# Kernel tuning notes

Hardware: AMD Instinct MI355X
Metric: run time of the kernel (lower is better)

## Reference

```python
import jax, jax.numpy as jnp
import numpy as np

B, P, Q, H = 8, 2048, 512, 1024


def setup_inputs() -> dict:
    key = jax.random.key(0)
    k1, k2, k3, k4, k5 = jax.random.split(key, 5)
    passage = jax.random.normal(k1, (B, P, H), dtype=jnp.float32)
    question = jax.random.normal(k2, (B, Q, H), dtype=jnp.float32)
    q_mask = jax.random.randint(k3, (B, Q), 0, 2, dtype=jnp.int32)
    # map_linear params (torch Linear: y = x @ W.T + b)
    bound = 1.0 / np.sqrt(H)
    map_W = jax.random.uniform(k4, (H, H), jnp.float32, -bound, bound)
    map_b = jax.random.uniform(k5, (H,), jnp.float32, -bound, bound)
    return {"passage": passage, "question": question, "q_mask": q_mask,
            "map_W": map_W, "map_b": map_b}


def reference(passage, question, q_mask, map_W, map_b):
    # scores: [B, P, Q]
    scores = jnp.einsum("bph,bqh->bpq", passage, question)
    mask = q_mask.astype(scores.dtype)[:, None, :]  # [B, 1, Q], broadcasts over P
    # multiplicative masked softmax + renormalize (memory_efficient=False path)
    a = jax.nn.softmax(scores * mask, axis=-1) * mask
    alpha = a / (jnp.sum(a, axis=-1, keepdims=True) + 1e-13)
    # attend: [B, P, H]
    out = jnp.einsum("bpq,bqh->bph", alpha, question)
    # fused linear + ReLU
    return jax.nn.relu(jnp.einsum("bph,oh->bpo", out, map_W) + map_b)
```

## Files before the change

### kernel.cpp

```cpp
#include <hip/hip_runtime.h>
#include <hip/hip_bf16.h>

typedef _Float16 f16;
typedef _Float16 f16x8 __attribute__((ext_vector_type(8)));
typedef _Float16 f16x4 __attribute__((ext_vector_type(4)));
typedef float f32x4 __attribute__((ext_vector_type(4)));
typedef int i32x4 __attribute__((ext_vector_type(4)));

#define B_ 8
#define P_ 2048
#define Q_ 512
#define H_ 1024

__device__ __forceinline__ void gload_lds16(const void* g, void* l) {
  __builtin_amdgcn_global_load_lds(
      (const __attribute__((address_space(1))) void*)g,
      (__attribute__((address_space(3))) void*)l, 16, 0, 0);
}

__global__ __launch_bounds__(256) void k_cvt16(const float* __restrict__ x,
                                               f16* __restrict__ y, int n4) {
  int i = blockIdx.x * blockDim.x + threadIdx.x;
  int stride = gridDim.x * blockDim.x;
  for (; i < n4; i += stride) {
    f32x4 v = ((const f32x4*)x)[i];
    f16x4 h;
#pragma unroll
    for (int j = 0; j < 4; ++j) h[j] = (f16)v[j];
    ((f16x4*)y)[i] = h;
  }
}

__global__ __launch_bounds__(256) void k_transpose(const float* __restrict__ q,
                                                   f16* __restrict__ qT,
                                                   f16* __restrict__ q16) {
  __shared__ float t[64][65];
  int b = blockIdx.z;
  int h0 = blockIdx.x * 64, q0 = blockIdx.y * 64;
  int tid = threadIdx.x;
  int c4 = (tid & 15) * 4;
  int r16 = tid >> 4;
  const float* src = q + ((long)b * Q_ + q0) * H_ + h0;
  f16* d16 = q16 + ((long)b * Q_ + q0) * H_ + h0;
#pragma unroll
  for (int i = 0; i < 4; ++i) {
    int r = r16 + i * 16;
    f32x4 v = *(const f32x4*)(src + (long)r * H_ + c4);
    f16x4 s;
#pragma unroll
    for (int j = 0; j < 4; ++j) s[j] = (f16)v[j];
    *(f16x4*)(d16 + (long)r * H_ + c4) = s;
    t[c4 + 0][r] = v[0];
    t[c4 + 1][r] = v[1];
    t[c4 + 2][r] = v[2];
    t[c4 + 3][r] = v[3];
  }
  __syncthreads();
  f16* dst = qT + ((long)b * H_ + h0) * Q_ + q0;
#pragma unroll
  for (int i = 0; i < 4; ++i) {
    int hr = r16 + i * 16;
    f16x4 o;
#pragma unroll
    for (int j = 0; j < 4; ++j) o[j] = (f16)t[hr][c4 + j];
    *(f16x4*)(dst + (long)hr * Q_ + c4) = o;
  }
}

__global__ __launch_bounds__(512, 2) void k_gemm1(
    const float* __restrict__ passage, const f16* __restrict__ q16,
    float* __restrict__ S) {
  constexpr int NT = H_ / 32;
  __shared__ __align__(16) f16 smem[40960];

  int orig = blockIdx.x;
  int wg = (orig & 7) * 32 + (orig >> 3);
  int bx = wg & 1, by = (wg >> 1) & 15, z = wg >> 5;
  int row0 = by * 128, col0 = bx * 256;

  int tid = threadIdx.x, wv = tid >> 6, lane = tid & 63;
  int fr = lane & 15, kq = lane >> 4;
  int wr = (wv >> 2) * 64, wc = (wv & 3) * 64;
  int swz = (kq ^ ((fr >> 1) & 3)) * 8;

  int ar = tid >> 2, ac = tid & 3;
  const float* gA = passage + ((long)(z * P_ + row0 + ar)) * H_ + ac * 8;
  int aw = ar * 32 + ((ac ^ ((ar >> 1) & 3)) * 8);

  const f16* gB = q16 + ((long)(z * Q_ + col0 + (tid >> 2))) * H_ +
                  (((tid & 3) ^ ((tid >> 3) & 3)) * 8);

  auto stageB = [&](int t) {
    const f16* g = gB + t * 32;
    f16* l = smem + 8192 + (t & 3) * 8192 + wv * 512;
    gload_lds16(g, l);
    gload_lds16(g + (long)128 * H_, l + 4096);
  };
  auto writeA = [&](int t, f32x4 lo, f32x4 hi) {
    f16x8 h;
#pragma unroll
    for (int j = 0; j < 4; ++j) {
      h[j] = (f16)lo[j];
      h[4 + j] = (f16)hi[j];
    }
    *(f16x8*)(smem + (t & 1) * 4096 + aw) = h;
  };

  f32x4 acc[4][4] = {};
  f32x4 a0lo, a0hi, a1lo, a1hi;

  a0lo = *(const f32x4*)(gA);
  a0hi = *(const f32x4*)(gA + 4);
  a1lo = *(const f32x4*)(gA + 32);
  a1hi = *(const f32x4*)(gA + 36);
  stageB(0);
  stageB(1);
  stageB(2);
  writeA(0, a0lo, a0hi);
  asm volatile("s_waitcnt vmcnt(4) lgkmcnt(0)" ::: "memory");
  __builtin_amdgcn_s_barrier();
  __builtin_amdgcn_sched_barrier(0);

#pragma unroll 4
  for (int t = 0; t < NT; ++t) {
    if (t + 2 < NT) {
      const float* g = gA + (t + 2) * 32;
      if (t & 1) {
        a1lo = *(const f32x4*)(g);
        a1hi = *(const f32x4*)(g + 4);
      } else {
        a0lo = *(const f32x4*)(g);
        a0hi = *(const f32x4*)(g + 4);
      }
    }
    if (t + 3 < NT) stageB(t + 3);
    f16x8 af[4], bf[4];
    const f16* Ab = smem + (t & 1) * 4096;
    const f16* Bb = smem + 8192 + (t & 3) * 8192;
#pragma unroll
    for (int m = 0; m < 4; ++m)
      af[m] = *(const f16x8*)(Ab + (wr + m * 16 + fr) * 32 + swz);
#pragma unroll
    for (int n = 0; n < 4; ++n)
      bf[n] = *(const f16x8*)(Bb + (wc + n * 16 + fr) * 32 + swz);
    if (t + 1 < NT)
      writeA(t + 1, (t & 1) ? a0lo : a1lo, (t & 1) ? a0hi : a1hi);
    __builtin_amdgcn_s_setprio(1);
#pragma unroll
    for (int m = 0; m < 4; ++m)
#pragma unroll
      for (int n = 0; n < 4; ++n)
        acc[m][n] = __builtin_amdgcn_mfma_f32_16x16x32_f16(af[m], bf[n],
                                                           acc[m][n], 0, 0, 0);
    __builtin_amdgcn_s_setprio(0);
    if (t <= NT - 4)
      asm volatile("s_waitcnt vmcnt(6) lgkmcnt(0)" ::: "memory");
    else if (t == NT - 3)
      asm volatile("s_waitcnt vmcnt(4) lgkmcnt(0)" ::: "memory");
    else
      asm volatile("s_waitcnt vmcnt(0) lgkmcnt(0)" ::: "memory");
    if (t < NT - 1) {
      __builtin_amdgcn_s_barrier();
      __builtin_amdgcn_sched_barrier(0);
    }
  }

  float* Sp = S + (long)z * P_ * Q_;
  int r0 = row0 + wr + (lane >> 4) * 4;
  int c0 = col0 + wc + fr;
#pragma unroll
  for (int m = 0; m < 4; ++m)
#pragma unroll
    for (int n = 0; n < 4; ++n)
#pragma unroll
      for (int j = 0; j < 4; ++j)
        Sp[(long)(r0 + m * 16 + j) * Q_ + c0 + n * 16] = acc[m][n][j];
}

__global__ __launch_bounds__(256) void k_softmax(const float* __restrict__ S,
                                                 const int* __restrict__ qmask,
                                                 f16* __restrict__ alpha) {
  int row = blockIdx.x * 4 + (threadIdx.x >> 6);
  int lane = threadIdx.x & 63;
  int b = row >> 11;
  const float* s = S + (long)row * Q_;
  const int* mp = qmask + b * Q_;
  f32x4 v0 = ((const f32x4*)s)[lane * 2];
  f32x4 v1 = ((const f32x4*)s)[lane * 2 + 1];
  i32x4 m0 = ((const i32x4*)mp)[lane * 2];
  i32x4 m1 = ((const i32x4*)mp)[lane * 2 + 1];
  float t[8], mf[8];
#pragma unroll
  for (int j = 0; j < 4; ++j) {
    mf[j] = (float)m0[j];     t[j] = v0[j] * mf[j];
    mf[4 + j] = (float)m1[j]; t[4 + j] = v1[j] * mf[4 + j];
  }
  float mx = t[0];
#pragma unroll
  for (int j = 1; j < 8; ++j) mx = fmaxf(mx, t[j]);
  for (int o = 32; o; o >>= 1) mx = fmaxf(mx, __shfl_xor(mx, o, 64));
  float e[8], Z = 0.f, Sm = 0.f;
#pragma unroll
  for (int j = 0; j < 8; ++j) {
    e[j] = expf(t[j] - mx);
    Z += e[j];
    Sm += e[j] * mf[j];
  }
  for (int o = 32; o; o >>= 1) {
    Z += __shfl_xor(Z, o, 64);
    Sm += __shfl_xor(Sm, o, 64);
  }
  float inv = 1.0f / (Sm + 1e-13f * Z);
  f16x8 out;
#pragma unroll
  for (int j = 0; j < 8; ++j) out[j] = (f16)(e[j] * mf[j] * inv);
  *(f16x8*)(alpha + (long)row * Q_ + lane * 8) = out;
}

template <int EPI, int NT>
__global__ __launch_bounds__(512, 2) void k_gemm256(
    const f16* __restrict__ A, const f16* __restrict__ Bm,
    void* __restrict__ Cv, const float* __restrict__ bias, int N, int gx,
    int gy, long sA, long sB, long sC) {
  constexpr int K = NT * 32;
  __shared__ __align__(16) f16 smem[65536];

  int nwg = gridDim.x;
  int orig = blockIdx.x;
  int wg = (orig & 7) * (nwg >> 3) + (orig >> 3);
  int bx = wg % gx;
  int tt = wg / gx;
  int by = tt % gy;
  int z = tt / gy;
  int row0 = by * 256, col0 = bx * 256;
  A += z * sA;
  Bm += z * sB;

  int tid = threadIdx.x, wv = tid >> 6, lane = tid & 63;

  bool isA = wv < 4;
  int u0 = (wv & 3) * 4;
  int srow = u0 * 16 + (lane >> 2);
  int sclog = ((lane & 3) ^ ((lane >> 3) & 3)) * 8;
  const f16* sbaseG = isA ? A + (long)(row0 + srow) * K + sclog
                          : Bm + (long)(col0 + srow) * K + sclog;
  int sbaseL = (isA ? 0 : 8192) + u0 * 512;

  auto stage = [&](int tile) {
    const f16* g = sbaseG + (long)tile * 32;
    f16* l = smem + (tile & 3) * 16384 + sbaseL;
#pragma unroll
    for (int j = 0; j < 4; ++j) gload_lds16(g + (long)j * 16 * K, l + j * 512);
  };

  int wr = (wv >> 2) * 128, wc = (wv & 3) * 64;
  int fr = lane & 15, kq = lane >> 4;
  int swz = (kq ^ ((fr >> 1) & 3)) * 8 + fr * 32;

  f32x4 acc[8][4] = {};
  auto compute = [&](int t) {
    const f16* bufA = smem + (t & 3) * 16384;
    const f16* bufB = bufA + 8192;
    f16x8 af[8], bfr[4];
#pragma unroll
    for (int m = 0; m < 8; ++m)
      af[m] = *(const f16x8*)(bufA + (wr + m * 16) * 32 + swz);
#pragma unroll
    for (int n = 0; n < 4; ++n)
      bfr[n] = *(const f16x8*)(bufB + (wc + n * 16) * 32 + swz);
#pragma unroll
    for (int m = 0; m < 8; ++m)
#pragma unroll
      for (int n = 0; n < 4; ++n)
        acc[m][n] = __builtin_amdgcn_mfma_f32_16x16x32_f16(af[m], bfr[n],
                                                           acc[m][n], 0, 0, 0);
  };

  stage(0);
  stage(1);
  stage(2);
  asm volatile("s_waitcnt vmcnt(8)" ::: "memory");
  __builtin_amdgcn_s_barrier();
  __builtin_amdgcn_sched_barrier(0);
  for (int t = 0; t < NT - 3; ++t) {
    stage(t + 3);
    compute(t);
    asm volatile("s_waitcnt vmcnt(8)" ::: "memory");
    __builtin_amdgcn_s_barrier();
    __builtin_amdgcn_sched_barrier(0);
  }
  compute(NT - 3);
  asm volatile("s_waitcnt vmcnt(4)" ::: "memory");
  __builtin_amdgcn_s_barrier();
  __builtin_amdgcn_sched_barrier(0);
  compute(NT - 2);
  asm volatile("s_waitcnt vmcnt(0)" ::: "memory");
  __builtin_amdgcn_s_barrier();
  __builtin_amdgcn_sched_barrier(0);
  compute(NT - 1);

  int r0 = row0 + wr + (lane >> 4) * 4;
  int c0 = col0 + wc + fr;
  if constexpr (EPI == 1) {
    f16* C = (f16*)Cv + z * sC;
#pragma unroll
    for (int m = 0; m < 8; ++m)
#pragma unroll
      for (int n = 0; n < 4; ++n)
#pragma unroll
        for (int j = 0; j < 4; ++j)
          C[(long)(r0 + m * 16 + j) * N + c0 + n * 16] = (f16)acc[m][n][j];
  } else {
    float* C = (float*)Cv;
#pragma unroll
    for (int n = 0; n < 4; ++n) {
      float bv = bias[c0 + n * 16];
#pragma unroll
      for (int m = 0; m < 8; ++m)
#pragma unroll
        for (int j = 0; j < 4; ++j) {
          float v = acc[m][n][j] + bv;
          __builtin_nontemporal_store(
              fmaxf(v, 0.f), &C[(long)(r0 + m * 16 + j) * N + c0 + n * 16]);
        }
    }
  }
}

extern "C" void kernel_launch(void* const* d_in, const int* in_sizes, int n_in,
                              void* d_out, int out_size, void* d_ws,
                              size_t ws_size, hipStream_t stream) {
  const float* passage = (const float*)d_in[0];
  const float* question = (const float*)d_in[1];
  const int* qmask = (const int*)d_in[2];
  const float* mapW = (const float*)d_in[3];
  const float* mapb = (const float*)d_in[4];

  char* ws = (char*)d_ws;
  size_t off = 0;
  auto alloc = [&](size_t bytes) {
    void* p = ws + off;
    off += (bytes + 255) & ~(size_t)255;
    return p;
  };
  f16* q16 = (f16*)alloc((size_t)B_ * Q_ * H_ * 2);
  f16* qT = (f16*)alloc((size_t)B_ * H_ * Q_ * 2);
  f16* w16 = (f16*)alloc((size_t)H_ * H_ * 2);
  f16* alpha = (f16*)alloc((size_t)B_ * P_ * Q_ * 2);
  f16* O = (f16*)alloc((size_t)B_ * P_ * H_ * 2);
  float* S = (float*)alloc((size_t)B_ * P_ * Q_ * 4);

  k_cvt16<<<512, 256, 0, stream>>>(mapW, w16, H_ * H_ / 4);
  k_transpose<<<dim3(H_ / 64, Q_ / 64, B_), 256, 0, stream>>>(question, qT,
                                                              q16);

  k_gemm1<<<256, 512, 0, stream>>>(passage, q16, S);

  k_softmax<<<B_ * P_ / 4, 256, 0, stream>>>(S, qmask, alpha);

  k_gemm256<1, Q_ / 32><<<256, 512, 0, stream>>>(
      alpha, qT, O, nullptr, H_, H_ / 256, P_ / 256, (long)P_ * Q_,
      (long)H_ * Q_, (long)P_ * H_);

  k_gemm256<2, H_ / 32><<<256, 512, 0, stream>>>(
      O, w16, d_out, mapb, H_, H_ / 256, (B_ * P_) / 256, 0, 0, 0);
}
```

Baseline: 118.1 us.

## Fuse partial masked softmax into score GEMM epilogue with split-row rescale

The score GEMM epilogue now computes a per-tile masked softmax: a row max reduced through LDS across the 256-column tile, the exponentials, and partial Z and masked sums. It writes unnormalized fp16 exponentials plus per-half-row (max, Z, Sm) partials instead of a full fp32 score matrix. A light rowscale kernel merges the two column-half partials and rescales alpha in place. This removes the fp32 S write and read (64MB each way) at the cost of extra epilogue syncs and LDS reductions in the GEMM. Storing unnormalized exponentials in fp16 before rescaling could change rounding slightly.

Result: slower. 123.5 us (+4.7%).

```diff
diff --git a/kernel.cpp b/kernel.cpp
--- a/kernel.cpp
+++ b/kernel.cpp
@@ -69,7 +69,8 @@
 
 __global__ __launch_bounds__(512, 2) void k_gemm1(
     const float* __restrict__ passage, const f16* __restrict__ q16,
-    float* __restrict__ S) {
+    const int* __restrict__ qmask, f16* __restrict__ alphaE,
+    float* __restrict__ part) {
   constexpr int NT = H_ / 32;
   __shared__ __align__(16) f16 smem[40960];
 
@@ -165,56 +166,102 @@
     }
   }
 
-  float* Sp = S + (long)z * P_ * Q_;
-  int r0 = row0 + wr + (lane >> 4) * 4;
-  int c0 = col0 + wc + fr;
+  __syncthreads();
+  float* red = (float*)smem;
+  float* red2 = red + 512;
+  const int* qm = qmask + z * Q_ + col0;
+  float mk[4];
+#pragma unroll
+  for (int n = 0; n < 4; ++n) mk[n] = (float)qm[wc + n * 16 + fr];
+
+  int rbase = wr + (lane >> 4) * 4;
+  float mxl[4][4];
 #pragma unroll
   for (int m = 0; m < 4; ++m)
 #pragma unroll
-    for (int n = 0; n < 4; ++n)
-#pragma unroll
-      for (int j = 0; j < 4; ++j)
-        Sp[(long)(r0 + m * 16 + j) * Q_ + c0 + n * 16] = acc[m][n][j];
-}
-
-__global__ __launch_bounds__(256) void k_softmax(const float* __restrict__ S,
-                                                 const int* __restrict__ qmask,
-                                                 f16* __restrict__ alpha) {
+    for (int j = 0; j < 4; ++j) {
+      float v = acc[m][0][j] * mk[0];
+#pragma unroll
+      for (int n = 1; n < 4; ++n) v = fmaxf(v, acc[m][n][j] * mk[n]);
+      v = fmaxf(v, __shfl_xor(v, 1, 64));
+      v = fmaxf(v, __shfl_xor(v, 2, 64));
+      v = fmaxf(v, __shfl_xor(v, 4, 64));
+      v = fmaxf(v, __shfl_xor(v, 8, 64));
+      if (fr == 0) red[(rbase + m * 16 + j) * 4 + (wv & 3)] = v;
+    }
+  __syncthreads();
+#pragma unroll
+  for (int m = 0; m < 4; ++m)
+#pragma unroll
+    for (int j = 0; j < 4; ++j) {
+      int r = rbase + m * 16 + j;
+      mxl[m][j] = fmaxf(fmaxf(red[r * 4], red[r * 4 + 1]),
+                        fmaxf(red[r * 4 + 2], red[r * 4 + 3]));
+    }
+#pragma unroll
+  for (int m = 0; m < 4; ++m)
+#pragma unroll
+    for (int j = 0; j < 4; ++j) {
+      float zs = 0.f, ss = 0.f;
+#pragma unroll
+      for (int n = 0; n < 4; ++n) {
+        float e = expf(acc[m][n][j] * mk[n] - mxl[m][j]);
+        acc[m][n][j] = e * mk[n];
+        zs += e;
+        ss += e * mk[n];
+      }
+      zs += __shfl_xor(zs, 1, 64); ss += __shfl_xor(ss, 1, 64);
+      zs += __shfl_xor(zs, 2, 64); ss += __shfl_xor(ss, 2, 64);
+      zs += __shfl_xor(zs, 4, 64); ss += __shfl_xor(ss, 4, 64);
+      zs += __shfl_xor(zs, 8, 64); ss += __shfl_xor(ss, 8, 64);
+      if (fr == 0) {
+        red2[((rbase + m * 16 + j) * 4 + (wv & 3)) * 2] = zs;
+        red2[((rbase + m * 16 + j) * 4 + (wv & 3)) * 2 + 1] = ss;
+      }
+    }
+  __syncthreads();
+  f16* ap = alphaE + ((long)(z * P_ + row0)) * Q_ + col0;
+#pragma unroll
+  for (int m = 0; m < 4; ++m)
+#pragma unroll
+    for (int j = 0; j < 4; ++j) {
+      int r = rbase + m * 16 + j;
+      if ((wv & 3) == 0 && fr == 0) {
+        float Z = 0.f, Sm = 0.f;
+#pragma unroll
+        for (int w = 0; w < 4; ++w) {
+          Z += red2[(r * 4 + w) * 2];
+          Sm += red2[(r * 4 + w) * 2 + 1];
+        }
+        float* pp = part + ((long)(z * 2 + bx) * P_ + row0 + r) * 4;
+        pp[0] = mxl[m][j];
+        pp[1] = Z;
+        pp[2] = Sm;
+      }
+#pragma unroll
+      for (int n = 0; n < 4; ++n)
+        ap[(long)r * Q_ + wc + n * 16 + fr] = (f16)acc[m][n][j];
+    }
+}
+
+__global__ __launch_bounds__(256) void k_rowscale(f16* __restrict__ alpha,
+                                                  const float* __restrict__ part) {
   int row = blockIdx.x * 4 + (threadIdx.x >> 6);
   int lane = threadIdx.x & 63;
-  int b = row >> 11;
-  const float* s = S + (long)row * Q_;
-  const int* mp = qmask + b * Q_;
-  f32x4 v0 = ((const f32x4*)s)[lane * 2];
-  f32x4 v1 = ((const f32x4*)s)[lane * 2 + 1];
-  i32x4 m0 = ((const i32x4*)mp)[lane * 2];
-  i32x4 m1 = ((const i32x4*)mp)[lane * 2 + 1];
-  float t[8], mf[8];
-#pragma unroll
-  for (int j = 0; j < 4; ++j) {
-    mf[j] = (float)m0[j];     t[j] = v0[j] * mf[j];
-    mf[4 + j] = (float)m1[j]; t[4 + j] = v1[j] * mf[4 + j];
-  }
-  float mx = t[0];
-#pragma unroll
-  for (int j = 1; j < 8; ++j) mx = fmaxf(mx, t[j]);
-  for (int o = 32; o; o >>= 1) mx = fmaxf(mx, __shfl_xor(mx, o, 64));
-  float e[8], Z = 0.f, Sm = 0.f;
-#pragma unroll
-  for (int j = 0; j < 8; ++j) {
-    e[j] = expf(t[j] - mx);
-    Z += e[j];
-    Sm += e[j] * mf[j];
-  }
-  for (int o = 32; o; o >>= 1) {
-    Z += __shfl_xor(Z, o, 64);
-    Sm += __shfl_xor(Sm, o, 64);
-  }
-  float inv = 1.0f / (Sm + 1e-13f * Z);
-  f16x8 out;
-#pragma unroll
-  for (int j = 0; j < 8; ++j) out[j] = (f16)(e[j] * mf[j] * inv);
-  *(f16x8*)(alpha + (long)row * Q_ + lane * 8) = out;
+  int z = row >> 11, pr = row & 2047;
+  const float* p0 = part + ((long)(z * 2 + 0) * P_ + pr) * 4;
+  const float* p1 = part + ((long)(z * 2 + 1) * P_ + pr) * 4;
+  float m0 = p0[0], Z0 = p0[1], S0 = p0[2];
+  float m1 = p1[0], Z1 = p1[1], S1 = p1[2];
+  float M = fmaxf(m0, m1);
+  float s0 = expf(m0 - M), s1 = expf(m1 - M);
+  float inv = 1.0f / (S0 * s0 + S1 * s1 + 1e-13f * (Z0 * s0 + Z1 * s1));
+  float sc = (lane < 32 ? s0 : s1) * inv;
+  f16* ap = alpha + (long)row * Q_ + lane * 8;
+  f16x8 v = *(f16x8*)ap;
+#pragma unroll
+  for (int j = 0; j < 8; ++j) v[j] = (f16)((float)v[j] * sc);
+  *(f16x8*)ap = v;
 }
 
 template <int EPI, int NT>
@@ -348,15 +395,15 @@
   f16* w16 = (f16*)alloc((size_t)H_ * H_ * 2);
   f16* alpha = (f16*)alloc((size_t)B_ * P_ * Q_ * 2);
   f16* O = (f16*)alloc((size_t)B_ * P_ * H_ * 2);
-  float* S = (float*)alloc((size_t)B_ * P_ * Q_ * 4);
+  float* part = (float*)alloc((size_t)B_ * 2 * P_ * 4 * 4);
 
   k_cvt16<<<512, 256, 0, stream>>>(mapW, w16, H_ * H_ / 4);
   k_transpose<<<dim3(H_ / 64, Q_ / 64, B_), 256, 0, stream>>>(question, qT,
                                                               q16);
 
-  k_gemm1<<<256, 512, 0, stream>>>(passage, q16, S);
-
-  k_softmax<<<B_ * P_ / 4, 256, 0, stream>>>(S, qmask, alpha);
+  k_gemm1<<<256, 512, 0, stream>>>(passage, q16, qmask, alpha, part);
+
+  k_rowscale<<<B_ * P_ / 4, 256, 0, stream>>>(alpha, part);
 
   k_gemm256<1, Q_ / 32><<<256, 512, 0, stream>>>(
       alpha, qT, O, nullptr, H_, H_ / 256, P_ / 256, (long)P_ * Q_,
```

## Restructure 256x256 GEMM to K=64 tiles with double buffering and prefetched fragments

Applied to the files above, without the earlier changes.

The 256x256 GEMM kernel now uses 64-wide K tiles with two LDS buffers instead of four 32-wide buffers, so there are half as many barriers per K loop. Each iteration loads all LDS fragments into registers first, waits, then issues the next stage's global-to-LDS loads so the buffer being read can be safely overwritten. The MFMA block runs under raised wave priority via s_setprio. The cost is a shallower prefetch (two stages instead of three) and more registers for the doubled fragments, which may reduce latency hiding or occupancy.

Result: slower. 151.6 us (+28.4%).

```diff
diff --git a/kernel.cpp b/kernel.cpp
--- a/kernel.cpp
+++ b/kernel.cpp
@@ -222,7 +222,7 @@
     const f16* __restrict__ A, const f16* __restrict__ Bm,
     void* __restrict__ Cv, const float* __restrict__ bias, int N, int gx,
     int gy, long sA, long sB, long sC) {
-  constexpr int K = NT * 32;
+  constexpr int K = NT * 64;
   __shared__ __align__(16) f16 smem[65536];
 
   int nwg = gridDim.x;
@@ -238,66 +238,79 @@
 
   int tid = threadIdx.x, wv = tid >> 6, lane = tid & 63;
 
-  bool isA = wv < 4;
-  int u0 = (wv & 3) * 4;
-  int srow = u0 * 16 + (lane >> 2);
-  int sclog = ((lane & 3) ^ ((lane >> 3) & 3)) * 8;
-  const f16* sbaseG = isA ? A + (long)(row0 + srow) * K + sclog
-                          : Bm + (long)(col0 + srow) * K + sclog;
-  int sbaseL = (isA ? 0 : 8192) + u0 * 512;
-
-  auto stage = [&](int tile) {
-    const f16* g = sbaseG + (long)tile * 32;
-    f16* l = smem + (tile & 3) * 16384 + sbaseL;
-#pragma unroll
-    for (int j = 0; j < 4; ++j) gload_lds16(g + (long)j * 16 * K, l + j * 512);
+  int rowR = tid >> 3;
+  int half = (tid >> 2) & 1;
+  int cl = (tid & 3) ^ ((rowR >> 1) & 3);
+  const f16* gAs = A + (long)(row0 + rowR) * K + half * 32 + cl * 8;
+  const f16* gBs = Bm + (long)(col0 + rowR) * K + half * 32 + cl * 8;
+
+  auto stage = [&](int t) {
+    f16* l = smem + (t & 1) * 32768 + tid * 8;
+    const f16* ga = gAs + (long)t * 64;
+    const f16* gb = gBs + (long)t * 64;
+#pragma unroll
+    for (int j = 0; j < 4; ++j)
+      gload_lds16(ga + (long)j * 64 * K, l + j * 4096);
+#pragma unroll
+    for (int j = 0; j < 4; ++j)
+      gload_lds16(gb + (long)j * 64 * K, l + 16384 + j * 4096);
   };
 
   int wr = (wv >> 2) * 128, wc = (wv & 3) * 64;
   int fr = lane & 15, kq = lane >> 4;
-  int swz = (kq ^ ((fr >> 1) & 3)) * 8 + fr * 32;
+  int swz = (kq ^ ((fr >> 1) & 3)) * 8;
 
   f32x4 acc[8][4] = {};
-  auto compute = [&](int t) {
-    const f16* bufA = smem + (t & 3) * 16384;
-    const f16* bufB = bufA + 8192;
-    f16x8 af[8], bfr[4];
-#pragma unroll
-    for (int m = 0; m < 8; ++m)
-      af[m] = *(const f16x8*)(bufA + (wr + m * 16) * 32 + swz);
-#pragma unroll
-    for (int n = 0; n < 4; ++n)
-      bfr[n] = *(const f16x8*)(bufB + (wc + n * 16) * 32 + swz);
-#pragma unroll
-    for (int m = 0; m < 8; ++m)
-#pragma unroll
-      for (int n = 0; n < 4; ++n)
-        acc[m][n] = __builtin_amdgcn_mfma_f32_16x16x32_f16(af[m], bfr[n],
-                                                           acc[m][n], 0, 0, 0);
-  };
 
   stage(0);
   stage(1);
-  stage(2);
   asm volatile("s_waitcnt vmcnt(8)" ::: "memory");
   __builtin_amdgcn_s_barrier();
   __builtin_amdgcn_sched_barrier(0);
-  for (int t = 0; t < NT - 3; ++t) {
-    stage(t + 3);
-    compute(t);
-    asm volatile("s_waitcnt vmcnt(8)" ::: "memory");
+#pragma unroll 2
+  for (int t = 0; t < NT; ++t) {
+    const f16* bufA = smem + (t & 1) * 32768;
+    const f16* bufB = bufA + 16384;
+    f16x8 af0[8], bf0[4], af1[8], bf1[4];
+#pragma unroll
+    for (int m = 0; m < 8; ++m)
+      af0[m] = *(const f16x8*)(bufA + (wr + m * 16 + fr) * 64 + swz);
+#pragma unroll
+    for (int n = 0; n < 4; ++n)
+      bf0[n] = *(const f16x8*)(bufB + (wc + n * 16 + fr) * 64 + swz);
+#pragma unroll
+    for (int m = 0; m < 8; ++m)
+      af1[m] = *(const f16x8*)(bufA + (wr + m * 16 + fr) * 64 + 32 + swz);
+#pragma unroll
+    for (int n = 0; n < 4; ++n)
+      bf1[n] = *(const f16x8*)(bufB + (wc + n * 16 + fr) * 64 + 32 + swz);
+    asm volatile("s_waitcnt lgkmcnt(0)" ::: "memory");
+    __builtin_amdgcn_sched_barrier(0);
     __builtin_amdgcn_s_barrier();
-    __builtin_amdgcn_sched_barrier(0);
-  }
-  compute(NT - 3);
-  asm volatile("s_waitcnt vmcnt(4)" ::: "memory");
-  __builtin_amdgcn_s_barrier();
-  __builtin_amdgcn_sched_barrier(0);
-  compute(NT - 2);
-  asm volatile("s_waitcnt vmcnt(0)" ::: "memory");
-  __builtin_amdgcn_s_barrier();
-  __builtin_amdgcn_sched_barrier(0);
-  compute(NT - 1);
+    if (t + 2 < NT) stage(t + 2);
+    __builtin_amdgcn_s_setprio(1);
+#pragma unroll
+    for (int m = 0; m < 8; ++m)
+#pragma unroll
+      for (int n = 0; n < 4; ++n)
+        acc[m][n] = __builtin_amdgcn_mfma_f32_16x16x32_f16(af0[m], bf0[n],
+                                                           acc[m][n], 0, 0, 0);
+#pragma unroll
+    for (int m = 0; m < 8; ++m)
+#pragma unroll
+      for (int n = 0; n < 4; ++n)
+        acc[m][n] = __builtin_amdgcn_mfma_f32_16x16x32_f16(af1[m], bf1[n],
+                                                           acc[m][n], 0, 0, 0);
+    __builtin_amdgcn_s_setprio(0);
+    if (t + 2 < NT)
+      asm volatile("s_waitcnt vmcnt(8)" ::: "memory");
+    else
+      asm volatile("s_waitcnt vmcnt(0)" ::: "memory");
+    if (t + 1 < NT) {
+      __builtin_amdgcn_s_barrier();
+      __builtin_amdgcn_sched_barrier(0);
+    }
+  }
 
   int r0 = row0 + wr + (lane >> 4) * 4;
   int c0 = col0 + wc + fr;
@@ -358,10 +371,10 @@
 
   k_softmax<<<B_ * P_ / 4, 256, 0, stream>>>(S, qmask, alpha);
 
-  k_gemm256<1, Q_ / 32><<<256, 512, 0, stream>>>(
+  k_gemm256<1, Q_ / 64><<<256, 512, 0, stream>>>(
       alpha, qT, O, nullptr, H_, H_ / 256, P_ / 256, (long)P_ * Q_,
       (long)H_ * Q_, (long)P_ * H_);
 
-  k_gemm256<2, H_ / 32><<<256, 512, 0, stream>>>(
+  k_gemm256<2, H_ / 64><<<256, 512, 0, stream>>>(
       O, w16, d_out, mapb, H_, H_ / 256, (B_ * P_) / 256, 0, 0, 0);
 }
```

## Shrink GEMM tiles to 256x128 with triple-buffered LDS and higher occupancy

Applied to the files above, without the earlier changes.

Changes the two f16 GEMMs from 256x256 to 256x128 output tiles, doubling the grid to 512 workgroups. The LDS pipeline drops from four 32 KB stages (three in flight) to three 24 KB slots (two in flight), and the launch-bounds occupancy hint rises from 2 to 4. s_setprio is raised around the MFMA block. Smaller tiles give more blocks and better wave occupancy across the 256 CUs, at the cost of lower arithmetic intensity per tile, more global and L2 traffic, and a shallower prefetch.

Result: no change. 119.4 us (+1.2%).

```diff
diff --git a/kernel.cpp b/kernel.cpp
--- a/kernel.cpp
+++ b/kernel.cpp
@@ -218,12 +218,13 @@
 }
 
 template <int EPI, int NT>
-__global__ __launch_bounds__(512, 2) void k_gemm256(
+__global__ __launch_bounds__(512, 4) void k_gemm256(
     const f16* __restrict__ A, const f16* __restrict__ Bm,
     void* __restrict__ Cv, const float* __restrict__ bias, int N, int gx,
     int gy, long sA, long sB, long sC) {
   constexpr int K = NT * 32;
-  __shared__ __align__(16) f16 smem[65536];
+  constexpr int SLOT = 12288;
+  __shared__ __align__(16) f16 smem[3 * SLOT];
 
   int nwg = gridDim.x;
   int orig = blockIdx.x;
@@ -232,72 +233,67 @@
   int tt = wg / gx;
   int by = tt % gy;
   int z = tt / gy;
-  int row0 = by * 256, col0 = bx * 256;
+  int row0 = by * 256, col0 = bx * 128;
   A += z * sA;
   Bm += z * sB;
 
   int tid = threadIdx.x, wv = tid >> 6, lane = tid & 63;
-
-  bool isA = wv < 4;
-  int u0 = (wv & 3) * 4;
-  int srow = u0 * 16 + (lane >> 2);
-  int sclog = ((lane & 3) ^ ((lane >> 3) & 3)) * 8;
-  const f16* sbaseG = isA ? A + (long)(row0 + srow) * K + sclog
-                          : Bm + (long)(col0 + srow) * K + sclog;
-  int sbaseL = (isA ? 0 : 8192) + u0 * 512;
-
-  auto stage = [&](int tile) {
-    const f16* g = sbaseG + (long)tile * 32;
-    f16* l = smem + (tile & 3) * 16384 + sbaseL;
-#pragma unroll
-    for (int j = 0; j < 4; ++j) gload_lds16(g + (long)j * 16 * K, l + j * 512);
-  };
-
-  int wr = (wv >> 2) * 128, wc = (wv & 3) * 64;
   int fr = lane & 15, kq = lane >> 4;
+
+  int scl = ((tid & 3) ^ ((tid >> 3) & 3)) * 8;
+  int R0 = tid >> 2;
+  const f16* g0 = A + (long)(row0 + R0) * K + scl;
+  const f16* g1 = A + (long)(row0 + 128 + R0) * K + scl;
+  const f16* g2 = Bm + (long)(col0 + R0) * K + scl;
+
+  auto stage = [&](int t) {
+    f16* l = smem + (t % 3) * SLOT + wv * 512;
+    gload_lds16(g0 + t * 32, l);
+    gload_lds16(g1 + t * 32, l + 4096);
+    gload_lds16(g2 + t * 32, l + 8192);
+  };
+
+  int wr = (wv >> 2) * 128, wc = (wv & 3) * 32;
   int swz = (kq ^ ((fr >> 1) & 3)) * 8 + fr * 32;
 
-  f32x4 acc[8][4] = {};
+  f32x4 acc[8][2] = {};
   auto compute = [&](int t) {
-    const f16* bufA = smem + (t & 3) * 16384;
+    const f16* bufA = smem + (t % 3) * SLOT;
     const f16* bufB = bufA + 8192;
-    f16x8 af[8], bfr[4];
+    f16x8 af[8], bfr[2];
 #pragma unroll
     for (int m = 0; m < 8; ++m)
       af[m] = *(const f16x8*)(bufA + (wr + m * 16) * 32 + swz);
 #pragma unroll
-    for (int n = 0; n < 4; ++n)
+    for (int n = 0; n < 2; ++n)
       bfr[n] = *(const f16x8*)(bufB + (wc + n * 16) * 32 + swz);
+    __builtin_amdgcn_s_setprio(1);
 #pragma unroll
     for (int m = 0; m < 8; ++m)
 #pragma unroll
-      for (int n = 0; n < 4; ++n)
+      for (int n = 0; n < 2; ++n)
         acc[m][n] = __builtin_amdgcn_mfma_f32_16x16x32_f16(af[m], bfr[n],
                                                            acc[m][n], 0, 0, 0);
+    __builtin_amdgcn_s_setprio(0);
   };
 
   stage(0);
   stage(1);
-  stage(2);
-  asm volatile("s_waitcnt vmcnt(8)" ::: "memory");
+  asm volatile("s_waitcnt vmcnt(3)" ::: "memory");
   __builtin_amdgcn_s_barrier();
   __builtin_amdgcn_sched_barrier(0);
-  for (int t = 0; t < NT - 3; ++t) {
-    stage(t + 3);
+  for (int t = 0; t < NT; ++t) {
+    if (t + 2 < NT) stage(t + 2);
     compute(t);
-    asm volatile("s_waitcnt vmcnt(8)" ::: "memory");
-    __builtin_amdgcn_s_barrier();
-    __builtin_amdgcn_sched_barrier(0);
-  }
-  compute(NT - 3);
-  asm volatile("s_waitcnt vmcnt(4)" ::: "memory");
-  __builtin_amdgcn_s_barrier();
-  __builtin_amdgcn_sched_barrier(0);
-  compute(NT - 2);
-  asm volatile("s_waitcnt vmcnt(0)" ::: "memory");
-  __builtin_amdgcn_s_barrier();
-  __builtin_amdgcn_sched_barrier(0);
-  compute(NT - 1);
+    if (t + 2 < NT)
+      asm volatile("s_waitcnt vmcnt(3)" ::: "memory");
+    else
+      asm volatile("s_waitcnt vmcnt(0)" ::: "memory");
+    if (t + 1 < NT) {
+      __builtin_amdgcn_s_barrier();
+      __builtin_amdgcn_sched_barrier(0);
+    }
+  }
 
   int r0 = row0 + wr + (lane >> 4) * 4;
   int c0 = col0 + wc + fr;
@@ -306,14 +302,14 @@
 #pragma unroll
     for (int m = 0; m < 8; ++m)
 #pragma unroll
-      for (int n = 0; n < 4; ++n)
+      for (int n = 0; n < 2; ++n)
 #pragma unroll
         for (int j = 0; j < 4; ++j)
           C[(long)(r0 + m * 16 + j) * N + c0 + n * 16] = (f16)acc[m][n][j];
   } else {
     float* C = (float*)Cv;
 #pragma unroll
-    for (int n = 0; n < 4; ++n) {
+    for (int n = 0; n < 2; ++n) {
       float bv = bias[c0 + n * 16];
 #pragma unroll
       for (int m = 0; m < 8; ++m)
@@ -358,10 +354,10 @@
 
   k_softmax<<<B_ * P_ / 4, 256, 0, stream>>>(S, qmask, alpha);
 
-  k_gemm256<1, Q_ / 32><<<256, 512, 0, stream>>>(
-      alpha, qT, O, nullptr, H_, H_ / 256, P_ / 256, (long)P_ * Q_,
+  k_gemm256<1, Q_ / 32><<<512, 512, 0, stream>>>(
+      alpha, qT, O, nullptr, H_, H_ / 128, P_ / 256, (long)P_ * Q_,
       (long)H_ * Q_, (long)P_ * H_);
 
-  k_gemm256<2, H_ / 32><<<256, 512, 0, stream>>>(
-      O, w16, d_out, mapb, H_, H_ / 256, (B_ * P_) / 256, 0, 0, 0);
-}
+  k_gemm256<2, H_ / 32><<<512, 512, 0, stream>>>(
+      O, w16, d_out, mapb, H_, H_ / 128, (B_ * P_) / 256, 0, 0, 0);
+}
```
